# Performance work log

Hardware: AMD Instinct MI355X
Metric: run time of the kernel (lower is better)

The kernel has to match this reference:

```python
import jax, jax.numpy as jnp
import numpy as np

ALPHA = 1000.0


def setup_inputs() -> dict:
    key = jax.random.key(0)
    ks = jax.random.split(key, 5)
    B, D_in, K = 8192, 2048, 256  # K = n_clusters = embed_dim (square cluster_reps)
    x = jax.random.normal(ks[0], (B, D_in), dtype=jnp.float32)
    W_enc = jax.random.normal(ks[1], (D_in, K), dtype=jnp.float32) * (1.0 / np.sqrt(D_in))
    b_enc = jnp.zeros((K,), dtype=jnp.float32)
    W_dec = jax.random.normal(ks[2], (K, D_in), dtype=jnp.float32) * (1.0 / np.sqrt(K))
    b_dec = jnp.zeros((D_in,), dtype=jnp.float32)
    cluster_reps = jax.random.normal(ks[3], (K, K), dtype=jnp.float32)
    return {"x": x, "W_enc": W_enc, "b_enc": b_enc, "W_dec": W_dec,
            "b_dec": b_dec, "cluster_reps": cluster_reps}


def reference(x, W_enc, b_enc, W_dec, b_dec, cluster_reps):
    # Autoencoder (linear MLP stand-in for the injected module)
    emb = x @ W_enc + b_enc                    # [B, K]
    reconstruction = emb @ W_dec + b_dec       # [B, D_in]

    # Squared Euclidean distance to each cluster rep, in GEMM form: [B, K]
    # dist[b, k] = ||emb_b||^2 - 2 emb_b . c_k + ||c_k||^2
    dist = (jnp.sum(emb * emb, axis=1, keepdims=True)
            - 2.0 * (emb @ cluster_reps.T)
            + jnp.sum(cluster_reps * cluster_reps, axis=1)[None, :])

    stack_dist = dist.T                        # [K, B] (matches torch.stack over clusters)
    min_dist = jnp.min(stack_dist, axis=0)     # [B]
    stack_exp = jnp.exp(-ALPHA * (stack_dist - min_dist[None, :]))  # stable softmin
    softmax = stack_exp / jnp.sum(stack_exp, axis=0, keepdims=True)
    weighted_dist = stack_dist * softmax       # [K, B]
    return weighted_dist, reconstruction
```

## Files before the change

### kernel.cpp

```cpp
#include <hip/hip_runtime.h>

#define ALPHA_F 1000.0f

typedef _Float16 half8 __attribute__((ext_vector_type(8)));
typedef float floatx4 __attribute__((ext_vector_type(4)));

__device__ __forceinline__ void gload_lds16(const void* g, void* l) {
    __builtin_amdgcn_global_load_lds(
        (const __attribute__((address_space(1))) unsigned int*)g,
        (__attribute__((address_space(3))) unsigned int*)l, 16, 0, 0);
}

__global__ __launch_bounds__(256) void prep(
    const float* __restrict__ W_enc, const float* __restrict__ W_dec,
    const float* __restrict__ creps,
    _Float16* __restrict__ Wh, _Float16* __restrict__ Wl,
    _Float16* __restrict__ Wdh,
    _Float16* __restrict__ Ch, _Float16* __restrict__ Cl,
    float* __restrict__ cnorm)
{
    const int bid = blockIdx.x;
    if (bid < 256) {
        const int q = bid * 256 + threadIdx.x;
        const int n = q & 255, k8 = q >> 8;
        const int k = k8 * 8;
        half8 h, l;
        #pragma unroll
        for (int i = 0; i < 8; ++i) {
            const float v = W_enc[(size_t)(k + i) * 256 + n] * 256.0f;
            const _Float16 hi = (_Float16)v;
            h[i] = hi;
            l[i] = (_Float16)(v - (float)hi);
        }
        const int kc = k >> 5, nt = n >> 4;
        const int lane = (n & 15) | ((k8 & 3) << 4);
        const size_t idx = (size_t)((kc * 16 + nt) * 64 + lane) * 8;
        *(half8*)(Wh + idx) = h;
        *(half8*)(Wl + idx) = l;
    } else if (bid < 512) {
        const int q = (bid - 256) * 256 + threadIdx.x;
        const int n = q & 2047, k8 = q >> 11;
        const int k = k8 * 8;
        half8 h;
        #pragma unroll
        for (int i = 0; i < 8; ++i) h[i] = (_Float16)W_dec[(size_t)(k + i) * 2048 + n];
        const int kc = k8 >> 2, nt = n >> 4;
        const int lane = (n & 15) | ((k8 & 3) << 4);
        *(half8*)(Wdh + (size_t)((kc * 128 + nt) * 64 + lane) * 8) = h;
    } else if (bid < 544) {
        const int q = (bid - 512) * 256 + threadIdx.x;
        const int n = q & 255, j8 = q >> 8;
        const int j = j8 * 8;
        half8 h, l;
        #pragma unroll
        for (int i = 0; i < 8; ++i) {
            const float v = creps[(size_t)n * 256 + j + i];
            const _Float16 hi = (_Float16)v;
            h[i] = hi;
            l[i] = (_Float16)((v - (float)hi) * 2048.0f);
        }
        const int jc = j >> 5, nt = n >> 4;
        const int lane = (n & 15) | ((j8 & 3) << 4);
        const size_t idx = (size_t)((jc * 16 + nt) * 64 + lane) * 8;
        *(half8*)(Ch + idx) = h;
        *(half8*)(Cl + idx) = l;
    } else {
        const int wid = threadIdx.x >> 6, lane = threadIdx.x & 63;
        const int row = (bid - 544) * 4 + wid;
        const float4 v = *(const float4*)(creps + (size_t)row * 256 + lane * 4);
        float s = v.x * v.x + v.y * v.y + v.z * v.z + v.w * v.w;
        #pragma unroll
        for (int off = 32; off >= 1; off >>= 1) s += __shfl_xor(s, off, 64);
        if (lane == 0) cnorm[row] = s;
    }
}

__global__ __launch_bounds__(256) void emb_gemm(
    const float* __restrict__ x, const _Float16* __restrict__ Wh,
    const _Float16* __restrict__ Wl, float* __restrict__ P)
{
    __shared__ _Float16 Ah[4 * 64 * 8], Al[4 * 64 * 8];
    __shared__ _Float16 Bh[16 * 64 * 8], Bl[16 * 64 * 8];
    const int t = threadIdx.x, lane = t & 63, w = t >> 6;
    const int kk = blockIdx.x;
    const int mb = blockIdx.y;
    const int m0 = mb * 64;

    const int am = t >> 2, q = t & 3;
    _Float16* AhW = Ah + (((am >> 4) * 64) + ((am & 15) | (q << 4))) * 8;
    _Float16* AlW = Al + (((am >> 4) * 64) + ((am & 15) | (q << 4))) * 8;
    const float* xP = x + (size_t)(m0 + am) * 2048 + kk * 512 + q * 8;

    floatx4 acc[4][4] = {};

    for (int it = 0; it < 16; ++it) {
        const float4 v0 = *(const float4*)(xP + it * 32);
        const float4 v1 = *(const float4*)(xP + it * 32 + 4);
        const int kc = kk * 16 + it;
        __syncthreads();
        const _Float16* bh_src = Wh + (size_t)kc * 16 * 512;
        const _Float16* bl_src = Wl + (size_t)kc * 16 * 512;
        #pragma unroll
        for (int i = 0; i < 4; ++i) {
            const int c = w * 4 + i;
            gload_lds16(bh_src + (size_t)c * 512 + lane * 8, Bh + c * 512);
            gload_lds16(bl_src + (size_t)c * 512 + lane * 8, Bl + c * 512);
        }
        half8 h8, l8;
        {
            const float vv[8] = {v0.x, v0.y, v0.z, v0.w, v1.x, v1.y, v1.z, v1.w};
            #pragma unroll
            for (int i = 0; i < 8; ++i) {
                const _Float16 hi = (_Float16)vv[i];
                h8[i] = hi;
                l8[i] = (_Float16)(vv[i] - (float)hi);
            }
        }
        *(half8*)AhW = h8;
        *(half8*)AlW = l8;
        __syncthreads();

        half8 ah[4], al[4], bh[4], bl[4];
        #pragma unroll
        for (int s = 0; s < 4; ++s) {
            ah[s] = *(const half8*)(Ah + (s * 64 + lane) * 8);
            al[s] = *(const half8*)(Al + (s * 64 + lane) * 8);
        }
        #pragma unroll
        for (int ni = 0; ni < 4; ++ni) {
            bh[ni] = *(const half8*)(Bh + ((w * 4 + ni) * 64 + lane) * 8);
            bl[ni] = *(const half8*)(Bl + ((w * 4 + ni) * 64 + lane) * 8);
        }
        #pragma unroll
        for (int mi = 0; mi < 4; ++mi) {
            #pragma unroll
            for (int ni = 0; ni < 4; ++ni) {
                acc[mi][ni] = __builtin_amdgcn_mfma_f32_16x16x32_f16(ah[mi], bl[ni], acc[mi][ni], 0, 0, 0);
                acc[mi][ni] = __builtin_amdgcn_mfma_f32_16x16x32_f16(al[mi], bh[ni], acc[mi][ni], 0, 0, 0);
                acc[mi][ni] = __builtin_amdgcn_mfma_f32_16x16x32_f16(ah[mi], bh[ni], acc[mi][ni], 0, 0, 0);
            }
        }
    }

    float* Pk = P + (size_t)kk * 2097152;
    #pragma unroll
    for (int mi = 0; mi < 4; ++mi) {
        #pragma unroll
        for (int ni = 0; ni < 4; ++ni) {
            const int col = w * 64 + ni * 16 + (lane & 15);
            const int rowBase = m0 + mi * 16 + (lane >> 4) * 4;
            #pragma unroll
            for (int r = 0; r < 4; ++r)
                Pk[(size_t)(rowBase + r) * 256 + col] = acc[mi][ni][r];
        }
    }
}

__global__ __launch_bounds__(256) void finalize(
    const float* __restrict__ P, const float* __restrict__ b_enc,
    _Float16* __restrict__ ehg, float* __restrict__ embf,
    float* __restrict__ enorm)
{
    const int t = threadIdx.x;
    const int b0 = blockIdx.x * 32;
    const int row = t >> 3, c8 = t & 7;
    const int grow = b0 + row;

    const float* p0 = P + (size_t)grow * 256 + c8 * 32;
    float4 v[8];
    #pragma unroll
    for (int i = 0; i < 8; ++i) v[i] = *(const float4*)(p0 + i * 4);
    #pragma unroll
    for (int kk = 1; kk < 4; ++kk) {
        const float* pk = p0 + (size_t)kk * 2097152;
        #pragma unroll
        for (int i = 0; i < 8; ++i) {
            const float4 a = *(const float4*)(pk + i * 4);
            v[i].x += a.x; v[i].y += a.y; v[i].z += a.z; v[i].w += a.w;
        }
    }
    const float inv = 1.0f / 256.0f;
    float e[32];
    float ssq = 0.0f;
    #pragma unroll
    for (int i = 0; i < 8; ++i) {
        const float4 b = *(const float4*)(b_enc + c8 * 32 + i * 4);
        e[i * 4 + 0] = v[i].x * inv + b.x;
        e[i * 4 + 1] = v[i].y * inv + b.y;
        e[i * 4 + 2] = v[i].z * inv + b.z;
        e[i * 4 + 3] = v[i].w * inv + b.w;
        ssq += e[i * 4 + 0] * e[i * 4 + 0];
        ssq += e[i * 4 + 1] * e[i * 4 + 1];
        ssq += e[i * 4 + 2] * e[i * 4 + 2];
        ssq += e[i * 4 + 3] * e[i * 4 + 3];
    }
    #pragma unroll
    for (int i = 0; i < 8; ++i) {
        float4 s4;
        s4.x = e[i * 4 + 0]; s4.y = e[i * 4 + 1];
        s4.z = e[i * 4 + 2]; s4.w = e[i * 4 + 3];
        *(float4*)(embf + (size_t)grow * 256 + c8 * 32 + i * 4) = s4;
    }
    #pragma unroll
    for (int oo = 0; oo < 4; ++oo) {
        const int q = c8 * 4 + oo;
        half8 h;
        #pragma unroll
        for (int i = 0; i < 8; ++i) h[i] = (_Float16)e[oo * 8 + i];
        const size_t idx = (size_t)(((grow >> 4) * 8 + (q >> 2)) * 64
                                    + ((grow & 15) | ((q & 3) << 4))) * 8;
        *(half8*)(ehg + idx) = h;
    }
    ssq += __shfl_xor(ssq, 1, 64);
    ssq += __shfl_xor(ssq, 2, 64);
    ssq += __shfl_xor(ssq, 4, 64);
    if (c8 == 0) enorm[grow] = ssq;
}

__global__ __launch_bounds__(256) void dist16(
    const float* __restrict__ embf, const _Float16* __restrict__ ch,
    const _Float16* __restrict__ cl, const float* __restrict__ enorm,
    const float* __restrict__ cnorm, float* __restrict__ out)
{
    __shared__ float D[16 * 257];
    __shared__ float MINV[16], SUMV[16];
    const int t = threadIdx.x, lane = t & 63, w = t >> 6;
    const int b0 = blockIdx.x * 16;
    const int arow16 = lane & 15, aoct = lane >> 4;

    floatx4 acc[4] = {}, accX[4] = {};
    for (int kc = 0; kc < 8; ++kc) {
        const float* fp = embf + (size_t)(b0 + arow16) * 256 + kc * 32 + aoct * 8;
        const float4 u0 = *(const float4*)(fp);
        const float4 u1 = *(const float4*)(fp + 4);
        const float vv[8] = {u0.x, u0.y, u0.z, u0.w, u1.x, u1.y, u1.z, u1.w};
        half8 ah, al;
        #pragma unroll
        for (int j = 0; j < 8; ++j) {
            const _Float16 hi = (_Float16)vv[j];
            ah[j] = hi;
            al[j] = (_Float16)((vv[j] - (float)hi) * 2048.0f);
        }
        #pragma unroll
        for (int ni = 0; ni < 4; ++ni) {
            const size_t bb = (size_t)((kc * 16 + (w * 4 + ni)) * 64 + lane) * 8;
            const half8 bh = *(const half8*)(ch + bb);
            const half8 bl = *(const half8*)(cl + bb);
            acc[ni]  = __builtin_amdgcn_mfma_f32_16x16x32_f16(ah, bh, acc[ni], 0, 0, 0);
            accX[ni] = __builtin_amdgcn_mfma_f32_16x16x32_f16(ah, bl, accX[ni], 0, 0, 0);
            accX[ni] = __builtin_amdgcn_mfma_f32_16x16x32_f16(al, bh, accX[ni], 0, 0, 0);
        }
    }

    const float invs = 1.0f / 2048.0f;
    #pragma unroll
    for (int ni = 0; ni < 4; ++ni) {
        const int k = w * 64 + ni * 16 + (lane & 15);
        const float cn = cnorm[k];
        #pragma unroll
        for (int r = 0; r < 4; ++r) {
            const int rl = (lane >> 4) * 4 + r;
            const float S = acc[ni][r] + accX[ni][r] * invs;
            D[rl * 257 + k] = enorm[b0 + rl] - 2.0f * S + cn;
        }
    }
    __syncthreads();

    #pragma unroll
    for (int rr = 0; rr < 4; ++rr) {
        const int r = w * 4 + rr;
        const float d0 = D[r * 257 + lane +   0];
        const float d1 = D[r * 257 + lane +  64];
        const float d2 = D[r * 257 + lane + 128];
        const float d3 = D[r * 257 + lane + 192];
        float mn = fminf(fminf(d0, d1), fminf(d2, d3));
        #pragma unroll
        for (int off = 32; off >= 1; off >>= 1) mn = fminf(mn, __shfl_xor(mn, off, 64));
        float s = expf(-ALPHA_F * (d0 - mn)) + expf(-ALPHA_F * (d1 - mn))
                + expf(-ALPHA_F * (d2 - mn)) + expf(-ALPHA_F * (d3 - mn));
        #pragma unroll
        for (int off = 32; off >= 1; off >>= 1) s += __shfl_xor(s, off, 64);
        if (lane == 0) { MINV[r] = mn; SUMV[r] = s; }
    }
    __syncthreads();

    const int b = t & 15, kg = t >> 4;
    const float mn = MINV[b], sv = SUMV[b];
    #pragma unroll
    for (int kk = 0; kk < 16; ++kk) {
        const int k = kk * 16 + kg;
        const float dv = D[b * 257 + k];
        out[(size_t)k * 8192 + b0 + b] = dv * expf(-ALPHA_F * (dv - mn)) / sv;
    }
}

__global__ __launch_bounds__(256) void recon_gemm(
    const _Float16* __restrict__ embh, const _Float16* __restrict__ Wdh,
    const float* __restrict__ b_dec, float* __restrict__ out)
{
    __shared__ _Float16 Ah[8 * 64 * 8];
    __shared__ _Float16 Bh[8 * 64 * 8];
    const int t = threadIdx.x, lane = t & 63, w = t >> 6;
    const int wm = w >> 1, wn = w & 1;
    const int nb = blockIdx.x, mb = blockIdx.y;

    floatx4 acc[4][4] = {};

    for (int kc = 0; kc < 8; ++kc) {
        __syncthreads();
        #pragma unroll
        for (int i = 0; i < 2; ++i) {
            const int c = w * 2 + i;
            gload_lds16(embh + (size_t)(((mb * 8 + c) * 8 + kc) * 64 + lane) * 8, Ah + c * 512);
            gload_lds16(Wdh + (size_t)((kc * 128 + nb * 8 + c) * 64 + lane) * 8, Bh + c * 512);
        }
        __syncthreads();
        half8 a[4], b[4];
        #pragma unroll
        for (int mi = 0; mi < 4; ++mi) a[mi] = *(const half8*)(Ah + ((wm * 4 + mi) * 64 + lane) * 8);
        #pragma unroll
        for (int ni = 0; ni < 4; ++ni) b[ni] = *(const half8*)(Bh + ((wn * 4 + ni) * 64 + lane) * 8);
        #pragma unroll
        for (int mi = 0; mi < 4; ++mi)
            #pragma unroll
            for (int ni = 0; ni < 4; ++ni)
                acc[mi][ni] = __builtin_amdgcn_mfma_f32_16x16x32_f16(a[mi], b[ni], acc[mi][ni], 0, 0, 0);
    }

    #pragma unroll
    for (int ni = 0; ni < 4; ++ni) {
        const int col = nb * 128 + (wn * 4 + ni) * 16 + (lane & 15);
        const float bias = b_dec[col];
        #pragma unroll
        for (int mi = 0; mi < 4; ++mi) {
            const int rowBase = mb * 128 + (wm * 4 + mi) * 16 + (lane >> 4) * 4;
            #pragma unroll
            for (int r = 0; r < 4; ++r)
                out[(size_t)(rowBase + r) * 2048 + col] = acc[mi][ni][r] + bias;
        }
    }
}

extern "C" void kernel_launch(void* const* d_in, const int* in_sizes, int n_in,
                              void* d_out, int out_size, void* d_ws, size_t ws_size,
                              hipStream_t stream) {
    const float* x     = (const float*)d_in[0];
    const float* W_enc = (const float*)d_in[1];
    const float* b_enc = (const float*)d_in[2];
    const float* W_dec = (const float*)d_in[3];
    const float* b_dec = (const float*)d_in[4];
    const float* creps = (const float*)d_in[5];

    float* out_w   = (float*)d_out;
    float* out_rec = out_w + (size_t)256 * 8192;
    float* P       = out_rec;

    float*     cnorm = (float*)d_ws;
    _Float16*  embh  = (_Float16*)(cnorm + 256);
    _Float16*  Whf   = embh + (size_t)8192 * 256;
    _Float16*  Wlf   = Whf + (size_t)2048 * 256;
    _Float16*  Wdh   = Wlf + (size_t)2048 * 256;
    _Float16*  crh   = Wdh + (size_t)256 * 2048;
    _Float16*  crl   = crh + (size_t)256 * 256;
    float*     enorm = (float*)(crl + (size_t)256 * 256);
    float*     embf  = enorm + 8192;

    prep<<<608, 256, 0, stream>>>(W_enc, W_dec, creps, Whf, Wlf, Wdh, crh, crl, cnorm);

    emb_gemm<<<dim3(4, 128), 256, 0, stream>>>(x, Whf, Wlf, P);

    finalize<<<256, 256, 0, stream>>>(P, b_enc, embh, embf, enorm);

    dist16<<<512, 256, 0, stream>>>(embf, crh, crl, enorm, cnorm, out_w);

    recon_gemm<<<dim3(16, 64), 256, 0, stream>>>(embh, Wdh, b_dec, out_rec);
}
```

Measured before the change: 207.6 us.

## Double-buffer LDS tiles in embedding and reconstruction GEMMs

Both the split-fp16 embedding GEMM and the reconstruction GEMM now use two LDS buffers. The next K-chunk is prefetched with global_load_lds, and in emb_gemm the next x values are loaded and split, while the current chunk's MFMAs run. This removes one barrier per iteration and is meant to hide global-load latency behind compute. In exchange LDS use doubles, which can lower occupancy. The prefetch writes into the other buffer after a single barrier, which relies on the async load completing before that barrier.

```diff
diff --git a/kernel.cpp b/kernel.cpp
--- a/kernel.cpp
+++ b/kernel.cpp
@@ -79,66 +79,95 @@
     const float* __restrict__ x, const _Float16* __restrict__ Wh,
     const _Float16* __restrict__ Wl, float* __restrict__ P)
 {
-    __shared__ _Float16 Ah[4 * 64 * 8], Al[4 * 64 * 8];
-    __shared__ _Float16 Bh[16 * 64 * 8], Bl[16 * 64 * 8];
+    __shared__ _Float16 Ah[2][4 * 64 * 8], Al[2][4 * 64 * 8];
+    __shared__ _Float16 Bh[2][16 * 64 * 8], Bl[2][16 * 64 * 8];
     const int t = threadIdx.x, lane = t & 63, w = t >> 6;
     const int kk = blockIdx.x;
     const int mb = blockIdx.y;
     const int m0 = mb * 64;
 
     const int am = t >> 2, q = t & 3;
-    _Float16* AhW = Ah + (((am >> 4) * 64) + ((am & 15) | (q << 4))) * 8;
-    _Float16* AlW = Al + (((am >> 4) * 64) + ((am & 15) | (q << 4))) * 8;
+    const int aoff = (((am >> 4) * 64) + ((am & 15) | (q << 4))) * 8;
     const float* xP = x + (size_t)(m0 + am) * 2048 + kk * 512 + q * 8;
 
     floatx4 acc[4][4] = {};
 
-    for (int it = 0; it < 16; ++it) {
-        const float4 v0 = *(const float4*)(xP + it * 32);
-        const float4 v1 = *(const float4*)(xP + it * 32 + 4);
-        const int kc = kk * 16 + it;
-        __syncthreads();
+    {
+        const float4 v0 = *(const float4*)(xP);
+        const float4 v1 = *(const float4*)(xP + 4);
+        const int kc = kk * 16;
         const _Float16* bh_src = Wh + (size_t)kc * 16 * 512;
         const _Float16* bl_src = Wl + (size_t)kc * 16 * 512;
         #pragma unroll
         for (int i = 0; i < 4; ++i) {
             const int c = w * 4 + i;
-            gload_lds16(bh_src + (size_t)c * 512 + lane * 8, Bh + c * 512);
-            gload_lds16(bl_src + (size_t)c * 512 + lane * 8, Bl + c * 512);
-        }
+            gload_lds16(bh_src + (size_t)c * 512 + lane * 8, &Bh[0][c * 512]);
+            gload_lds16(bl_src + (size_t)c * 512 + lane * 8, &Bl[0][c * 512]);
+        }
+        const float vv[8] = {v0.x, v0.y, v0.z, v0.w, v1.x, v1.y, v1.z, v1.w};
         half8 h8, l8;
-        {
-            const float vv[8] = {v0.x, v0.y, v0.z, v0.w, v1.x, v1.y, v1.z, v1.w};
+        #pragma unroll
+        for (int i = 0; i < 8; ++i) {
+            const _Float16 hi = (_Float16)vv[i];
+            h8[i] = hi;
+            l8[i] = (_Float16)(vv[i] - (float)hi);
+        }
+        *(half8*)(&Ah[0][aoff]) = h8;
+        *(half8*)(&Al[0][aoff]) = l8;
+        __syncthreads();
+    }
+
+    for (int it = 0; it < 16; ++it) {
+        const int buf = it & 1;
+
+        float4 n0, n1;
+        if (it < 15) {
+            n0 = *(const float4*)(xP + (it + 1) * 32);
+            n1 = *(const float4*)(xP + (it + 1) * 32 + 4);
+            const int kc = kk * 16 + it + 1;
+            const _Float16* bh_src = Wh + (size_t)kc * 16 * 512;
+            const _Float16* bl_src = Wl + (size_t)kc * 16 * 512;
+            #pragma unroll
+            for (int i = 0; i < 4; ++i) {
+                const int c = w * 4 + i;
+                gload_lds16(bh_src + (size_t)c * 512 + lane * 8, &Bh[buf ^ 1][c * 512]);
+                gload_lds16(bl_src + (size_t)c * 512 + lane * 8, &Bl[buf ^ 1][c * 512]);
+            }
+        }
+
+        half8 ah[4], al[4], bh[4], bl[4];
+        #pragma unroll
+        for (int s = 0; s < 4; ++s) {
+            ah[s] = *(const half8*)(&Ah[buf][(s * 64 + lane) * 8]);
+            al[s] = *(const half8*)(&Al[buf][(s * 64 + lane) * 8]);
+        }
+        #pragma unroll
+        for (int ni = 0; ni < 4; ++ni) {
+            bh[ni] = *(const half8*)(&Bh[buf][((w * 4 + ni) * 64 + lane) * 8]);
+            bl[ni] = *(const half8*)(&Bl[buf][((w * 4 + ni) * 64 + lane) * 8]);
+        }
+        #pragma unroll
+        for (int mi = 0; mi < 4; ++mi) {
+            #pragma unroll
+            for (int ni = 0; ni < 4; ++ni) {
+                acc[mi][ni] = __builtin_amdgcn_mfma_f32_16x16x32_f16(ah[mi], bl[ni], acc[mi][ni], 0, 0, 0);
+                acc[mi][ni] = __builtin_amdgcn_mfma_f32_16x16x32_f16(al[mi], bh[ni], acc[mi][ni], 0, 0, 0);
+                acc[mi][ni] = __builtin_amdgcn_mfma_f32_16x16x32_f16(ah[mi], bh[ni], acc[mi][ni], 0, 0, 0);
+            }
+        }
+
+        if (it < 15) {
+            const float vv[8] = {n0.x, n0.y, n0.z, n0.w, n1.x, n1.y, n1.z, n1.w};
+            half8 h8, l8;
             #pragma unroll
             for (int i = 0; i < 8; ++i) {
                 const _Float16 hi = (_Float16)vv[i];
                 h8[i] = hi;
                 l8[i] = (_Float16)(vv[i] - (float)hi);
             }
-        }
-        *(half8*)AhW = h8;
-        *(half8*)AlW = l8;
-        __syncthreads();
-
-        half8 ah[4], al[4], bh[4], bl[4];
-        #pragma unroll
-        for (int s = 0; s < 4; ++s) {
-            ah[s] = *(const half8*)(Ah + (s * 64 + lane) * 8);
-            al[s] = *(const half8*)(Al + (s * 64 + lane) * 8);
-        }
-        #pragma unroll
-        for (int ni = 0; ni < 4; ++ni) {
-            bh[ni] = *(const half8*)(Bh + ((w * 4 + ni) * 64 + lane) * 8);
-            bl[ni] = *(const half8*)(Bl + ((w * 4 + ni) * 64 + lane) * 8);
-        }
-        #pragma unroll
-        for (int mi = 0; mi < 4; ++mi) {
-            #pragma unroll
-            for (int ni = 0; ni < 4; ++ni) {
-                acc[mi][ni] = __builtin_amdgcn_mfma_f32_16x16x32_f16(ah[mi], bl[ni], acc[mi][ni], 0, 0, 0);
-                acc[mi][ni] = __builtin_amdgcn_mfma_f32_16x16x32_f16(al[mi], bh[ni], acc[mi][ni], 0, 0, 0);
-                acc[mi][ni] = __builtin_amdgcn_mfma_f32_16x16x32_f16(ah[mi], bh[ni], acc[mi][ni], 0, 0, 0);
-            }
+            *(half8*)(&Ah[buf ^ 1][aoff]) = h8;
+            *(half8*)(&Al[buf ^ 1][aoff]) = l8;
+            __syncthreads();
         }
     }
 
@@ -298,33 +327,45 @@
     const _Float16* __restrict__ embh, const _Float16* __restrict__ Wdh,
     const float* __restrict__ b_dec, float* __restrict__ out)
 {
-    __shared__ _Float16 Ah[8 * 64 * 8];
-    __shared__ _Float16 Bh[8 * 64 * 8];
+    __shared__ _Float16 Ah[2][8 * 64 * 8];
+    __shared__ _Float16 Bh[2][8 * 64 * 8];
     const int t = threadIdx.x, lane = t & 63, w = t >> 6;
     const int wm = w >> 1, wn = w & 1;
     const int nb = blockIdx.x, mb = blockIdx.y;
 
     floatx4 acc[4][4] = {};
 
+    #pragma unroll
+    for (int i = 0; i < 2; ++i) {
+        const int c = w * 2 + i;
+        gload_lds16(embh + (size_t)(((mb * 8 + c) * 8 + 0) * 64 + lane) * 8, &Ah[0][c * 512]);
+        gload_lds16(Wdh + (size_t)((0 * 128 + nb * 8 + c) * 64 + lane) * 8, &Bh[0][c * 512]);
+    }
+    __syncthreads();
+
     for (int kc = 0; kc < 8; ++kc) {
-        __syncthreads();
-        #pragma unroll
-        for (int i = 0; i < 2; ++i) {
-            const int c = w * 2 + i;
-            gload_lds16(embh + (size_t)(((mb * 8 + c) * 8 + kc) * 64 + lane) * 8, Ah + c * 512);
-            gload_lds16(Wdh + (size_t)((kc * 128 + nb * 8 + c) * 64 + lane) * 8, Bh + c * 512);
-        }
-        __syncthreads();
+        const int buf = kc & 1;
+        if (kc < 7) {
+            #pragma unroll
+            for (int i = 0; i < 2; ++i) {
+                const int c = w * 2 + i;
+                gload_lds16(embh + (size_t)(((mb * 8 + c) * 8 + (kc + 1)) * 64 + lane) * 8,
+                            &Ah[buf ^ 1][c * 512]);
+                gload_lds16(Wdh + (size_t)(((kc + 1) * 128 + nb * 8 + c) * 64 + lane) * 8,
+                            &Bh[buf ^ 1][c * 512]);
+            }
+        }
         half8 a[4], b[4];
         #pragma unroll
-        for (int mi = 0; mi < 4; ++mi) a[mi] = *(const half8*)(Ah + ((wm * 4 + mi) * 64 + lane) * 8);
-        #pragma unroll
-        for (int ni = 0; ni < 4; ++ni) b[ni] = *(const half8*)(Bh + ((wn * 4 + ni) * 64 + lane) * 8);
+        for (int mi = 0; mi < 4; ++mi) a[mi] = *(const half8*)(&Ah[buf][((wm * 4 + mi) * 64 + lane) * 8]);
+        #pragma unroll
+        for (int ni = 0; ni < 4; ++ni) b[ni] = *(const half8*)(&Bh[buf][((wn * 4 + ni) * 64 + lane) * 8]);
         #pragma unroll
         for (int mi = 0; mi < 4; ++mi)
             #pragma unroll
             for (int ni = 0; ni < 4; ++ni)
                 acc[mi][ni] = __builtin_amdgcn_mfma_f32_16x16x32_f16(a[mi], b[ni], acc[mi][ni], 0, 0, 0);
+        if (kc < 7) __syncthreads();
     }
 
     #pragma unroll
```

After: 200.8 us. 3.3% less time.
